# Kernel optimization log

Hardware: AMD Instinct MI355X
Metric: run time of the kernel (lower is better)

Reference implementation:

```python
import jax, jax.numpy as jnp
import numpy as np

N = 4096
TAU = 0.2          # args.tau relaxation temperature
EPS = 1e-10        # numerical guard for logit of clamped probs


def setup_inputs() -> dict:
    key = jax.random.key(0)
    k1, k2, k3 = jax.random.split(key, 3)
    r = jax.random.uniform(k1, (N, N))
    ori_adj = jnp.where(r < 0.005, -1.0, jnp.where(r < 0.01, 1.0, 0.0)).astype(jnp.float32)
    # nn.init.uniform_(change_links_prob, 0.0, 0.001)
    change_links_prob = jax.random.uniform(k2, (N, N), minval=0.0, maxval=0.001, dtype=jnp.float32)
    # uniform noise for the RelaxedBernoulli logistic reparameterization
    u = jax.random.uniform(k3, (N, N), minval=1e-6, maxval=1.0 - 1e-6, dtype=jnp.float32)
    return {"ori_adj": ori_adj, "change_links_prob": change_links_prob, "u": u}


def reference(ori_adj, change_links_prob, u):
    # --- get_modified_adj: RelaxedBernoulliStraightThrough(tau, clamp(p,0,1)).rsample() ---
    p = jnp.clip(change_links_prob, EPS, 1.0 - EPS)      # torch.clamp(p, 0, 1) + logit guard
    logits = jnp.log(p) - jnp.log1p(-p)
    noise = jnp.log(u) - jnp.log1p(-u)                   # logistic noise
    soft = jax.nn.sigmoid((logits + noise) / TAU)        # relaxed sample
    hard = jnp.round(soft)                               # quantized sample
    change_prob = soft + jax.lax.stop_gradient(hard - soft)  # straight-through
    mod_adj = ori_adj + change_prob * (-2.0 * ori_adj)   # ori_adj * (1 - 2*b)

    # --- balance_degree_directed(mod_adj) ---
    # torch.diag(matrix) returns the diagonal VECTOR, broadcast-subtracted per row (faithful).
    A = mod_adj + mod_adj.T - jnp.diag(mod_adj)
    A_abs = jnp.abs(A)
    tr3 = jnp.einsum('ij,jk,ki->', A, A, A)              # trace(A @ A @ A)
    tr3_abs = jnp.einsum('ij,jk,ki->', A_abs, A_abs, A_abs)
    balance = 0.5 * (1.0 + tr3 / tr3_abs)
    return mod_adj, balance
```

## Files before the change

kernel.cpp:

```cpp
#include <hip/hip_runtime.h>
#include <hip/hip_bf16.h>
#include <cstdint>
#include <cstddef>

#define N 4096
#define NN ((size_t)N * (size_t)N)

typedef int int4v __attribute__((ext_vector_type(4)));

__device__ inline void async16(const void* g, void* lds) {
    __builtin_amdgcn_global_load_lds(
        (const __attribute__((address_space(1))) void*)g,
        (__attribute__((address_space(3))) void*)lds, 16, 0, 0);
}

__global__ void mod_kernel(const float4* __restrict__ ori,
                           const float4* __restrict__ clp,
                           const float4* __restrict__ u,
                           float4* __restrict__ out,
                           double* __restrict__ accs) {
    size_t i = (size_t)blockIdx.x * blockDim.x + threadIdx.x;
    float4 o4 = ori[i], p4 = clp[i], u4 = u[i];
    float po[4] = {p4.x, p4.y, p4.z, p4.w};
    float uo[4] = {u4.x, u4.y, u4.z, u4.w};
    float oo[4] = {o4.x, o4.y, o4.z, o4.w};
    float ro[4];
    #pragma unroll
    for (int k = 0; k < 4; ++k) {
        float p = fminf(fmaxf(po[k], 1e-10f), 1.0f - 1e-10f);
        float logits = logf(p) - log1pf(-p);
        float uu = uo[k];
        float noise = logf(uu) - log1pf(-uu);
        float y = (logits + noise) / 0.2f;
        float soft = 1.0f / (1.0f + expf(-y));
        float hard = rintf(soft);
        float o = oo[k];
        ro[k] = o + hard * (-2.0f * o);
    }
    out[i] = make_float4(ro[0], ro[1], ro[2], ro[3]);
    if (blockIdx.x == 0 && threadIdx.x < 2) accs[threadIdx.x] = 0.0;
}

__global__ void build_A8(const float* __restrict__ mod,
                         signed char* __restrict__ A,
                         signed char* __restrict__ AT,
                         signed char* __restrict__ Aa,
                         signed char* __restrict__ ATa) {
    __shared__ float tji[32][33];
    __shared__ float dloc[32];
    __shared__ signed char cv[32][36];
    const int bi = blockIdx.x * 32;
    const int bj = blockIdx.y * 32;
    const int tx = threadIdx.x;
    const int ty = threadIdx.y;
    {
        const float4 v = *(const float4*)&mod[(size_t)(bj + ty) * N + bi + tx * 4];
        tji[ty][tx * 4 + 0] = v.x; tji[ty][tx * 4 + 1] = v.y;
        tji[ty][tx * 4 + 2] = v.z; tji[ty][tx * 4 + 3] = v.w;
    }
    if (tx == 0) dloc[ty] = mod[(size_t)(bj + ty) * N + bj + ty];
    __syncthreads();
    const float4 mv = *(const float4*)&mod[(size_t)(bi + ty) * N + bj + tx * 4];
    float m4[4] = {mv.x, mv.y, mv.z, mv.w};
    int pkA = 0, pkAa = 0;
    #pragma unroll
    for (int k = 0; k < 4; ++k) {
        int jl = tx * 4 + k;
        float a = m4[k] + tji[jl][ty] - dloc[jl];
        int ai = (int)a;
        cv[ty][jl] = (signed char)ai;
        int au = ai < 0 ? -ai : ai;
        pkA  |= (ai & 255) << (8 * k);
        pkAa |= (au & 255) << (8 * k);
    }
    *(int*)&A [(size_t)(bi + ty) * N + bj + tx * 4] = pkA;
    *(int*)&Aa[(size_t)(bi + ty) * N + bj + tx * 4] = pkAa;
    __syncthreads();
    int pkT = 0, pkTa = 0;
    #pragma unroll
    for (int k = 0; k < 4; ++k) {
        int il = tx * 4 + k;
        int v = cv[il][ty];
        int va = v < 0 ? -v : v;
        pkT  |= (v  & 255) << (8 * k);
        pkTa |= (va & 255) << (8 * k);
    }
    *(int*)&AT [(size_t)(bj + ty) * N + bi + tx * 4] = pkT;
    *(int*)&ATa[(size_t)(bj + ty) * N + bi + tx * 4] = pkTa;
}

__global__ __launch_bounds__(256) void gemm_trace_i8(const signed char* __restrict__ Ag,
                                                     const signed char* __restrict__ ATg,
                                                     const signed char* __restrict__ Aag,
                                                     const signed char* __restrict__ ATag,
                                                     double* __restrict__ accs) {
    __shared__ int4v As4[1024];
    __shared__ int4v Bs4[1024];
    __shared__ int red[4];
    const int z = blockIdx.z;
    const signed char* Asrc = z ? Aag  : Ag;
    const signed char* Bsrc = z ? ATag : ATg;
    const int i0 = blockIdx.y * 128;
    const int k0 = blockIdx.x * 128;
    const int t = threadIdx.x;
    const int lane = t & 63;
    const int wave = t >> 6;
    const int quad = lane >> 4;
    const int col  = lane & 15;
    const int wr = (wave >> 1) * 64;
    const int wc = (wave & 1) * 64;
    signed char* Asc = (signed char*)As4;
    signed char* Bsc = (signed char*)Bs4;

    const int r0 = t >> 2;
    const int s0 = t & 3;
    const int c0 = s0 ^ ((r0 >> 1) & 3);
    const signed char* gA = Asrc + (size_t)(i0 + r0) * N + c0 * 16;
    const signed char* gB = Bsrc + (size_t)(k0 + r0) * N + c0 * 16;
    const int ldst = t * 16;

    int4v acc[4][4];
    #pragma unroll
    for (int a = 0; a < 4; ++a)
        #pragma unroll
        for (int b = 0; b < 4; ++b)
            acc[a][b] = (int4v){0, 0, 0, 0};

    const int fsw = ((quad ^ ((col >> 1) & 3)) << 4);

    for (int kb = 0; kb < N; kb += 128) {
        __syncthreads();
        const signed char* ga = gA + kb;
        const signed char* gb = gB + kb;
        async16(ga,              Asc + ldst);
        async16(ga + 64 * N,     Asc + 4096  + ldst);
        async16(ga + 64,         Asc + 8192  + ldst);
        async16(ga + 64 * N + 64, Asc + 12288 + ldst);
        async16(gb,              Bsc + ldst);
        async16(gb + 64 * N,     Bsc + 4096  + ldst);
        async16(gb + 64,         Bsc + 8192  + ldst);
        async16(gb + 64 * N + 64, Bsc + 12288 + ldst);
        __syncthreads();
        int4v af0[4], af1[4], bf0[4], bf1[4];
        #pragma unroll
        for (int tr = 0; tr < 4; ++tr) {
            const int ra = (wr + tr * 16 + col) << 6;
            af0[tr] = *(const int4v*)(Asc + ra + fsw);
            af1[tr] = *(const int4v*)(Asc + 8192 + ra + fsw);
        }
        #pragma unroll
        for (int tc = 0; tc < 4; ++tc) {
            const int rb = (wc + tc * 16 + col) << 6;
            bf0[tc] = *(const int4v*)(Bsc + rb + fsw);
            bf1[tc] = *(const int4v*)(Bsc + 8192 + rb + fsw);
        }
        #pragma unroll
        for (int tr = 0; tr < 4; ++tr)
            #pragma unroll
            for (int tc = 0; tc < 4; ++tc)
                acc[tr][tc] = __builtin_amdgcn_mfma_i32_16x16x64_i8(af0[tr], bf0[tc], acc[tr][tc], 0, 0, 0);
        #pragma unroll
        for (int tr = 0; tr < 4; ++tr)
            #pragma unroll
            for (int tc = 0; tc < 4; ++tc)
                acc[tr][tc] = __builtin_amdgcn_mfma_i32_16x16x64_i8(af1[tr], bf1[tc], acc[tr][tc], 0, 0, 0);
    }

    int part = 0;
    #pragma unroll
    for (int tr = 0; tr < 4; ++tr) {
        #pragma unroll
        for (int tc = 0; tc < 4; ++tc) {
            const int ib = i0 + wr + tr * 16 + quad * 4;
            const int kk = k0 + wc + tc * 16 + col;
            #pragma unroll
            for (int r = 0; r < 4; ++r)
                part += acc[tr][tc][r] * (int)Bsrc[(size_t)(ib + r) * N + kk];
        }
    }
    #pragma unroll
    for (int off = 32; off > 0; off >>= 1)
        part += __shfl_down(part, off, 64);
    if (lane == 0) red[wave] = part;
    __syncthreads();
    if (t == 0) {
        int tot = red[0] + red[1] + red[2] + red[3];
        atomicAdd(&accs[z], (double)tot);
    }
}

__global__ void finalize_kernel(const double* __restrict__ accs, float* __restrict__ out) {
    out[NN] = (float)(0.5 * (1.0 + accs[0] / accs[1]));
}

extern "C" void kernel_launch(void* const* d_in, const int* in_sizes, int n_in,
                              void* d_out, int out_size, void* d_ws, size_t ws_size,
                              hipStream_t stream) {
    const float* ori = (const float*)d_in[0];
    const float* clp = (const float*)d_in[1];
    const float* u   = (const float*)d_in[2];
    float* out = (float*)d_out;
    char* ws = (char*)d_ws;
    signed char* A8   = (signed char*)ws;
    signed char* AT8  = (signed char*)(ws + NN);
    signed char* Aa8  = (signed char*)(ws + 2 * NN);
    signed char* ATa8 = (signed char*)(ws + 3 * NN);
    double*      accs = (double*)(ws + 4 * NN);

    mod_kernel<<<dim3((unsigned)(NN / 1024)), 256, 0, stream>>>(
        (const float4*)ori, (const float4*)clp, (const float4*)u, (float4*)out, accs);
    build_A8<<<dim3(N / 32, N / 32), dim3(8, 32), 0, stream>>>(out, A8, AT8, Aa8, ATa8);
    gemm_trace_i8<<<dim3(N / 128, N / 128, 2), 256, 0, stream>>>(A8, AT8, Aa8, ATa8, accs);
    finalize_kernel<<<1, 1, 0, stream>>>(accs, out);
}
```

Before: 435.0 us.

## Fuse mod computation with int8 A build; switch GEMM to 32x32x32 MFMA

The elementwise relaxed-Bernoulli kernel and the symmetric int8 A/AT builder become one kernel. It processes mirrored 32x32 tile pairs (only the lower-triangle blocks launch work), and a small pre-kernel computes the diagonal. This removes the write-then-reread of the fp32 mod_adj and the redundant transpose reads. Separately, the trace GEMM swaps 16x16x64 i8 MFMAs for 32x32x32 i8 MFMAs with a 2x2 accumulator tiling, which changes LDS fragment reads and the epilogue index mapping. Half the blocks in the fused grid exit immediately, and the epilogue layout mapping must match the 32x32 MFMA output layout.

```diff
diff --git a/kernel.cpp b/kernel.cpp
--- a/kernel.cpp
+++ b/kernel.cpp
@@ -6,7 +6,8 @@
 #define N 4096
 #define NN ((size_t)N * (size_t)N)
 
-typedef int int4v __attribute__((ext_vector_type(4)));
+typedef int int4v  __attribute__((ext_vector_type(4)));
+typedef int int16v __attribute__((ext_vector_type(16)));
 
 __device__ inline void async16(const void* g, void* lds) {
     __builtin_amdgcn_global_load_lds(
@@ -14,79 +15,96 @@
         (__attribute__((address_space(3))) void*)lds, 16, 0, 0);
 }
 
-__global__ void mod_kernel(const float4* __restrict__ ori,
-                           const float4* __restrict__ clp,
-                           const float4* __restrict__ u,
-                           float4* __restrict__ out,
-                           double* __restrict__ accs) {
-    size_t i = (size_t)blockIdx.x * blockDim.x + threadIdx.x;
-    float4 o4 = ori[i], p4 = clp[i], u4 = u[i];
-    float po[4] = {p4.x, p4.y, p4.z, p4.w};
-    float uo[4] = {u4.x, u4.y, u4.z, u4.w};
-    float oo[4] = {o4.x, o4.y, o4.z, o4.w};
-    float ro[4];
+__device__ inline float mod_elem(float p, float uu, float o) {
+    p = fminf(fmaxf(p, 1e-10f), 1.0f - 1e-10f);
+    float logits = logf(p) - log1pf(-p);
+    float noise  = logf(uu) - log1pf(-uu);
+    float y = (logits + noise) / 0.2f;
+    float soft = 1.0f / (1.0f + expf(-y));
+    float hard = rintf(soft);
+    return o + hard * (-2.0f * o);
+}
+
+__global__ void diag_kernel(const float* __restrict__ ori, const float* __restrict__ clp,
+                            const float* __restrict__ u, float* __restrict__ diag,
+                            double* __restrict__ accs) {
+    int j = blockIdx.x * blockDim.x + threadIdx.x;
+    size_t idx = (size_t)j * N + j;
+    diag[j] = mod_elem(clp[idx], u[idx], ori[idx]);
+    if (blockIdx.x == 0 && threadIdx.x < 2) accs[threadIdx.x] = 0.0;
+}
+
+__global__ __launch_bounds__(256) void fused_mod_A(
+        const float* __restrict__ ori, const float* __restrict__ clp,
+        const float* __restrict__ u, const float* __restrict__ diag,
+        float* __restrict__ out,
+        signed char* __restrict__ A, signed char* __restrict__ AT,
+        signed char* __restrict__ Aa, signed char* __restrict__ ATa) {
+    const int bx = blockIdx.x, by = blockIdx.y;
+    if (bx > by) return;
+    const int bi = bx * 32, bj = by * 32;
+    __shared__ float mij[32][33];
+    __shared__ float mji[32][33];
+    const int t = threadIdx.x;
+    const int r  = t >> 3;
+    const int c4 = (t & 7) * 4;
+    {
+        size_t idx = (size_t)(bi + r) * N + bj + c4;
+        float4 p4 = *(const float4*)&clp[idx];
+        float4 u4 = *(const float4*)&u[idx];
+        float4 o4 = *(const float4*)&ori[idx];
+        float m0 = mod_elem(p4.x, u4.x, o4.x);
+        float m1 = mod_elem(p4.y, u4.y, o4.y);
+        float m2 = mod_elem(p4.z, u4.z, o4.z);
+        float m3 = mod_elem(p4.w, u4.w, o4.w);
+        *(float4*)&out[idx] = make_float4(m0, m1, m2, m3);
+        mij[r][c4] = m0; mij[r][c4 + 1] = m1; mij[r][c4 + 2] = m2; mij[r][c4 + 3] = m3;
+        if (bx != by) {
+            size_t idx2 = (size_t)(bj + r) * N + bi + c4;
+            float4 q4 = *(const float4*)&clp[idx2];
+            float4 v4 = *(const float4*)&u[idx2];
+            float4 w4 = *(const float4*)&ori[idx2];
+            float n0 = mod_elem(q4.x, v4.x, w4.x);
+            float n1 = mod_elem(q4.y, v4.y, w4.y);
+            float n2 = mod_elem(q4.z, v4.z, w4.z);
+            float n3 = mod_elem(q4.w, v4.w, w4.w);
+            *(float4*)&out[idx2] = make_float4(n0, n1, n2, n3);
+            mji[r][c4] = n0; mji[r][c4 + 1] = n1; mji[r][c4 + 2] = n2; mji[r][c4 + 3] = n3;
+        } else {
+            mji[r][c4] = m0; mji[r][c4 + 1] = m1; mji[r][c4 + 2] = m2; mji[r][c4 + 3] = m3;
+        }
+    }
+    __syncthreads();
+    const float djr = diag[bj + r];
+    const float dir = diag[bi + r];
+    int pkA = 0, pkAa = 0, pkT = 0, pkTa = 0;
+    int qkA = 0, qkAa = 0, qkT = 0, qkTa = 0;
     #pragma unroll
     for (int k = 0; k < 4; ++k) {
-        float p = fminf(fmaxf(po[k], 1e-10f), 1.0f - 1e-10f);
-        float logits = logf(p) - log1pf(-p);
-        float uu = uo[k];
-        float noise = logf(uu) - log1pf(-uu);
-        float y = (logits + noise) / 0.2f;
-        float soft = 1.0f / (1.0f + expf(-y));
-        float hard = rintf(soft);
-        float o = oo[k];
-        ro[k] = o + hard * (-2.0f * o);
-    }
-    out[i] = make_float4(ro[0], ro[1], ro[2], ro[3]);
-    if (blockIdx.x == 0 && threadIdx.x < 2) accs[threadIdx.x] = 0.0;
-}
-
-__global__ void build_A8(const float* __restrict__ mod,
-                         signed char* __restrict__ A,
-                         signed char* __restrict__ AT,
-                         signed char* __restrict__ Aa,
-                         signed char* __restrict__ ATa) {
-    __shared__ float tji[32][33];
-    __shared__ float dloc[32];
-    __shared__ signed char cv[32][36];
-    const int bi = blockIdx.x * 32;
-    const int bj = blockIdx.y * 32;
-    const int tx = threadIdx.x;
-    const int ty = threadIdx.y;
-    {
-        const float4 v = *(const float4*)&mod[(size_t)(bj + ty) * N + bi + tx * 4];
-        tji[ty][tx * 4 + 0] = v.x; tji[ty][tx * 4 + 1] = v.y;
-        tji[ty][tx * 4 + 2] = v.z; tji[ty][tx * 4 + 3] = v.w;
-    }
-    if (tx == 0) dloc[ty] = mod[(size_t)(bj + ty) * N + bj + ty];
-    __syncthreads();
-    const float4 mv = *(const float4*)&mod[(size_t)(bi + ty) * N + bj + tx * 4];
-    float m4[4] = {mv.x, mv.y, mv.z, mv.w};
-    int pkA = 0, pkAa = 0;
-    #pragma unroll
-    for (int k = 0; k < 4; ++k) {
-        int jl = tx * 4 + k;
-        float a = m4[k] + tji[jl][ty] - dloc[jl];
-        int ai = (int)a;
-        cv[ty][jl] = (signed char)ai;
-        int au = ai < 0 ? -ai : ai;
+        const int c = c4 + k;
+        const float x = mij[r][c], xt = mij[c][r];
+        const float y = mji[r][c], yt = mji[c][r];
+        int ai = (int)(x + yt - diag[bj + c]);
+        int ti = (int)(xt + y - djr);
         pkA  |= (ai & 255) << (8 * k);
-        pkAa |= (au & 255) << (8 * k);
-    }
-    *(int*)&A [(size_t)(bi + ty) * N + bj + tx * 4] = pkA;
-    *(int*)&Aa[(size_t)(bi + ty) * N + bj + tx * 4] = pkAa;
-    __syncthreads();
-    int pkT = 0, pkTa = 0;
-    #pragma unroll
-    for (int k = 0; k < 4; ++k) {
-        int il = tx * 4 + k;
-        int v = cv[il][ty];
-        int va = v < 0 ? -v : v;
-        pkT  |= (v  & 255) << (8 * k);
-        pkTa |= (va & 255) << (8 * k);
-    }
-    *(int*)&AT [(size_t)(bj + ty) * N + bi + tx * 4] = pkT;
-    *(int*)&ATa[(size_t)(bj + ty) * N + bi + tx * 4] = pkTa;
+        pkAa |= ((ai < 0 ? -ai : ai) & 255) << (8 * k);
+        pkT  |= (ti & 255) << (8 * k);
+        pkTa |= ((ti < 0 ? -ti : ti) & 255) << (8 * k);
+        int mi = (int)(y + xt - diag[bi + c]);
+        int si = (int)(yt + x - dir);
+        qkA  |= (mi & 255) << (8 * k);
+        qkAa |= ((mi < 0 ? -mi : mi) & 255) << (8 * k);
+        qkT  |= (si & 255) << (8 * k);
+        qkTa |= ((si < 0 ? -si : si) & 255) << (8 * k);
+    }
+    const size_t o1 = (size_t)(bi + r) * N + bj + c4;
+    const size_t o2 = (size_t)(bj + r) * N + bi + c4;
+    *(int*)&A [o1] = pkA;  *(int*)&Aa [o1] = pkAa;
+    *(int*)&AT[o2] = pkT;  *(int*)&ATa[o2] = pkTa;
+    if (bx != by) {
+        *(int*)&A [o2] = qkA;  *(int*)&Aa [o2] = qkAa;
+        *(int*)&AT[o1] = qkT;  *(int*)&ATa[o1] = qkTa;
+    }
 }
 
 __global__ __launch_bounds__(256) void gemm_trace_i8(const signed char* __restrict__ Ag,
@@ -105,77 +123,80 @@
     const int t = threadIdx.x;
     const int lane = t & 63;
     const int wave = t >> 6;
-    const int quad = lane >> 4;
-    const int col  = lane & 15;
     const int wr = (wave >> 1) * 64;
     const int wc = (wave & 1) * 64;
+    const int m32 = lane & 31;
+    const int kg  = lane >> 5;
     signed char* Asc = (signed char*)As4;
     signed char* Bsc = (signed char*)Bs4;
 
     const int r0 = t >> 2;
-    const int s0 = t & 3;
-    const int c0 = s0 ^ ((r0 >> 1) & 3);
+    const int c0 = (t & 3) ^ ((r0 >> 1) & 3);
     const signed char* gA = Asrc + (size_t)(i0 + r0) * N + c0 * 16;
     const signed char* gB = Bsrc + (size_t)(k0 + r0) * N + c0 * 16;
     const int ldst = t * 16;
 
-    int4v acc[4][4];
-    #pragma unroll
-    for (int a = 0; a < 4; ++a)
+    int16v acc[2][2];
+    #pragma unroll
+    for (int a = 0; a < 2; ++a)
         #pragma unroll
-        for (int b = 0; b < 4; ++b)
-            acc[a][b] = (int4v){0, 0, 0, 0};
-
-    const int fsw = ((quad ^ ((col >> 1) & 3)) << 4);
+        for (int b = 0; b < 2; ++b)
+            acc[a][b] = (int16v)(0);
 
     for (int kb = 0; kb < N; kb += 128) {
         __syncthreads();
         const signed char* ga = gA + kb;
         const signed char* gb = gB + kb;
-        async16(ga,              Asc + ldst);
-        async16(ga + 64 * N,     Asc + 4096  + ldst);
-        async16(ga + 64,         Asc + 8192  + ldst);
+        async16(ga,               Asc + ldst);
+        async16(ga + 64 * N,      Asc + 4096  + ldst);
+        async16(ga + 64,          Asc + 8192  + ldst);
         async16(ga + 64 * N + 64, Asc + 12288 + ldst);
-        async16(gb,              Bsc + ldst);
-        async16(gb + 64 * N,     Bsc + 4096  + ldst);
-        async16(gb + 64,         Bsc + 8192  + ldst);
+        async16(gb,               Bsc + ldst);
+        async16(gb + 64 * N,      Bsc + 4096  + ldst);
+        async16(gb + 64,          Bsc + 8192  + ldst);
         async16(gb + 64 * N + 64, Bsc + 12288 + ldst);
         __syncthreads();
-        int4v af0[4], af1[4], bf0[4], bf1[4];
         #pragma unroll
-        for (int tr = 0; tr < 4; ++tr) {
-            const int ra = (wr + tr * 16 + col) << 6;
-            af0[tr] = *(const int4v*)(Asc + ra + fsw);
-            af1[tr] = *(const int4v*)(Asc + 8192 + ra + fsw);
+        for (int half = 0; half < 2; ++half) {
+            const int hb = half * 8192;
+            #pragma unroll
+            for (int q = 0; q < 2; ++q) {
+                int4v af[2], bf[2];
+                #pragma unroll
+                for (int tr = 0; tr < 2; ++tr) {
+                    const int row = wr + tr * 32 + m32;
+                    const int slot = (q * 2 + kg) ^ ((row >> 1) & 3);
+                    af[tr] = *(const int4v*)(Asc + hb + (row << 6) + (slot << 4));
+                }
+                #pragma unroll
+                for (int tc = 0; tc < 2; ++tc) {
+                    const int row = wc + tc * 32 + m32;
+                    const int slot = (q * 2 + kg) ^ ((row >> 1) & 3);
+                    bf[tc] = *(const int4v*)(Bsc + hb + (row << 6) + (slot << 4));
+                }
+                #pragma unroll
+                for (int tr = 0; tr < 2; ++tr)
+                    #pragma unroll
+                    for (int tc = 0; tc < 2; ++tc)
+                        acc[tr][tc] = __builtin_amdgcn_mfma_i32_32x32x32_i8(
+                            af[tr], bf[tc], acc[tr][tc], 0, 0, 0);
+            }
         }
+    }
+
+    int part = 0;
+    const int rbase = 4 * kg;
+    #pragma unroll
+    for (int tr = 0; tr < 2; ++tr) {
         #pragma unroll
-        for (int tc = 0; tc < 4; ++tc) {
-            const int rb = (wc + tc * 16 + col) << 6;
-            bf0[tc] = *(const int4v*)(Bsc + rb + fsw);
-            bf1[tc] = *(const int4v*)(Bsc + 8192 + rb + fsw);
-        }
-        #pragma unroll
-        for (int tr = 0; tr < 4; ++tr)
+        for (int tc = 0; tc < 2; ++tc) {
+            const int ib = i0 + wr + tr * 32;
+            const int kk = k0 + wc + tc * 32 + m32;
             #pragma unroll
-            for (int tc = 0; tc < 4; ++tc)
-                acc[tr][tc] = __builtin_amdgcn_mfma_i32_16x16x64_i8(af0[tr], bf0[tc], acc[tr][tc], 0, 0, 0);
-        #pragma unroll
-        for (int tr = 0; tr < 4; ++tr)
-            #pragma unroll
-            for (int tc = 0; tc < 4; ++tc)
-                acc[tr][tc] = __builtin_amdgcn_mfma_i32_16x16x64_i8(af1[tr], bf1[tc], acc[tr][tc], 0, 0, 0);
-    }
-
-    int part = 0;
-    #pragma unroll
-    for (int tr = 0; tr < 4; ++tr) {
-        #pragma unroll
-        for (int tc = 0; tc < 4; ++tc) {
-            const int ib = i0 + wr + tr * 16 + quad * 4;
-            const int kk = k0 + wc + tc * 16 + col;
-            #pragma unroll
-            for (int r = 0; r < 4; ++r)
-                part += acc[tr][tc][r] * (int)Bsrc[(size_t)(ib + r) * N + kk];
+            for (int reg = 0; reg < 16; ++reg) {
+                const int row = (reg & 3) + 8 * (reg >> 2) + rbase;
+                part += acc[tr][tc][reg] * (int)Bsrc[(size_t)(ib + row) * N + kk];
+            }
         }
     }
     #pragma unroll
@@ -205,11 +226,12 @@
     signed char* AT8  = (signed char*)(ws + NN);
     signed char* Aa8  = (signed char*)(ws + 2 * NN);
     signed char* ATa8 = (signed char*)(ws + 3 * NN);
-    double*      accs = (double*)(ws + 4 * NN);
-
-    mod_kernel<<<dim3((unsigned)(NN / 1024)), 256, 0, stream>>>(
-        (const float4*)ori, (const float4*)clp, (const float4*)u, (float4*)out, accs);
-    build_A8<<<dim3(N / 32, N / 32), dim3(8, 32), 0, stream>>>(out, A8, AT8, Aa8, ATa8);
+    float*       diag = (float*)(ws + 4 * NN);
+    double*      accs = (double*)(ws + 4 * NN + 4096 * 4);
+
+    diag_kernel<<<dim3(16), 256, 0, stream>>>(ori, clp, u, diag, accs);
+    fused_mod_A<<<dim3(N / 32, N / 32), 256, 0, stream>>>(ori, clp, u, diag, out,
+                                                          A8, AT8, Aa8, ATa8);
     gemm_trace_i8<<<dim3(N / 128, N / 128, 2), 256, 0, stream>>>(A8, AT8, Aa8, ATa8, accs);
     finalize_kernel<<<1, 1, 0, stream>>>(accs, out);
 }
```

After: 448.7 us. 1.03x slower.
